# Performance work log

Hardware: AMD Instinct MI355X
Metric: run time of the kernel (lower is better)

The kernel has to match this reference:

```python
import jax, jax.numpy as jnp
import numpy as np

B, N, C = 4, 2048, 1152
H = 16
DH = C // H  # 72
EPS = 1e-6
THETA = 10000.0


def _rms_norm(x, w):
    # per-head RMSNorm in fp32, matching LlamaRMSNorm
    xf = x.astype(jnp.float32)
    var = jnp.mean(xf * xf, axis=-1, keepdims=True)
    return (w * (xf * jax.lax.rsqrt(var + EPS)).astype(x.dtype))


def _rope_cos_sin(n, dh, dtype):
    half = dh // 2
    inv_freq = 1.0 / (THETA ** (jnp.arange(0, half, dtype=jnp.float32) / half))
    ang = jnp.arange(n, dtype=jnp.float32)[:, None] * inv_freq[None, :]  # [N, half]
    return jnp.cos(ang).astype(dtype), jnp.sin(ang).astype(dtype)


def _apply_rope(x, cos, sin):
    # x: [B,H,N,DH]; rotate-half style
    half = x.shape[-1] // 2
    x1, x2 = x[..., :half], x[..., half:]
    return jnp.concatenate([x1 * cos - x2 * sin, x2 * cos + x1 * sin], axis=-1)


def setup_inputs() -> dict:
    key = jax.random.key(0)
    ks = jax.random.split(key, 3)
    x = jax.random.normal(ks[0], (B, N, C), dtype=jnp.float32)
    w_qkv = jax.random.normal(ks[1], (3 * C, C), dtype=jnp.float32) * (C ** -0.5)
    w_proj = jax.random.normal(ks[2], (C, C), dtype=jnp.float32) * (C ** -0.5)
    b_proj = jnp.zeros((C,), dtype=jnp.float32)
    q_norm_w = jnp.ones((DH,), dtype=jnp.float32)
    k_norm_w = jnp.ones((DH,), dtype=jnp.float32)
    return {"x": x, "w_qkv": w_qkv, "w_proj": w_proj, "b_proj": b_proj,
            "q_norm_w": q_norm_w, "k_norm_w": k_norm_w}


def reference(x, w_qkv, w_proj, b_proj, q_norm_w, k_norm_w):
    b, n, c = x.shape
    # QKV projection (no bias)
    qkv = jnp.einsum('bnc,dc->bnd', x, w_qkv)  # [B,N,3C]
    qkv = qkv.reshape(b, n, 3, H, DH).transpose(2, 0, 3, 1, 4)  # [3,B,H,N,DH]
    q, k, v = qkv[0], qkv[1], qkv[2]
    # RoPE on q, k
    cos, sin = _rope_cos_sin(n, DH, x.dtype)  # [N, DH/2]
    q = _apply_rope(q, cos, sin)
    k = _apply_rope(k, cos, sin)
    # per-head QK RMSNorm
    q = _rms_norm(q, q_norm_w)
    k = _rms_norm(k, k_norm_w)
    # scaled dot-product attention
    scale = DH ** -0.5
    attn = jax.nn.softmax(jnp.einsum('bhqd,bhkd->bhqk', q, k) * scale, axis=-1)
    out = jnp.einsum('bhqk,bhkd->bhqd', attn, v)  # [B,H,N,DH]
    out = out.transpose(0, 2, 1, 3).reshape(b, n, c)
    return jnp.einsum('bnc,dc->bnd', out, w_proj) + b_proj
```

## Files before the change

kernel.cpp:

```cpp
#include <hip/hip_runtime.h>
#include <stdint.h>

#define BATCH 4
#define NSEQ  2048
#define CDIM  1152
#define HB    16
#define DHD   72
#define D3    3456
#define NT    8192

typedef __attribute__((ext_vector_type(8))) short short8;
typedef __attribute__((ext_vector_type(8))) unsigned short u16x8;
typedef __attribute__((ext_vector_type(4))) unsigned short u16x4;
typedef __attribute__((ext_vector_type(4))) float f32x4;

__device__ __forceinline__ float bf2f(unsigned short u) {
  return __uint_as_float(((unsigned)u) << 16);
}
__device__ __forceinline__ unsigned short f2bf(float f) {
  unsigned u = __float_as_uint(f);
  u += 0x7FFF + ((u >> 16) & 1);
  return (unsigned short)(u >> 16);
}
__device__ __forceinline__ unsigned short f2bf_ru(float f) {
  return (unsigned short)((__float_as_uint(f) + 0x8000u) >> 16);
}

__device__ __forceinline__ void gload_lds16(const unsigned short* g, unsigned short* l) {
  __builtin_amdgcn_global_load_lds(
      (const __attribute__((address_space(1))) void*)g,
      (__attribute__((address_space(3))) void*)l, 16, 0, 0);
}

#define XN    ((size_t)NT * CDIM)
#define WQN   ((size_t)D3 * CDIM)
#define WPN   ((size_t)CDIM * CDIM)
#define CVT_CHUNKS ((XN + WQN + WPN) / 4)

__global__ __launch_bounds__(256) void cvt_bf16(
    const float* __restrict__ x, const float* __restrict__ wq,
    const float* __restrict__ wp, unsigned short* __restrict__ xb,
    unsigned short* __restrict__ wqb, unsigned short* __restrict__ wpb) {
  size_t c = (size_t)blockIdx.x * 256 + threadIdx.x;
  if (c >= CVT_CHUNKS) return;
  const float* src;
  unsigned short* dst;
  size_t e = c * 4;
  if (e < XN) { src = x + e; dst = xb + e; }
  else if (e < XN + WQN) { src = wq + (e - XN); dst = wqb + (e - XN); }
  else { src = wp + (e - XN - WQN); dst = wpb + (e - XN - WQN); }
  f32x4 v = *(const f32x4*)src;
  u16x4 r;
#pragma unroll
  for (int i = 0; i < 4; i++) r[i] = f2bf(v[i]);
  *(u16x4*)dst = r;
}

template <int SCATTER>
__global__ __launch_bounds__(256) void gemm_bt(
    const unsigned short* __restrict__ A, const unsigned short* __restrict__ Bt,
    const float* __restrict__ bias, void* __restrict__ Cout,
    unsigned short* __restrict__ Vt, int M, int Dn, int K) {
  __shared__ __attribute__((aligned(16))) unsigned short sA[128 * 32];
  __shared__ __attribute__((aligned(16))) unsigned short sB[128 * 32];

  const int tid  = threadIdx.x;
  const int lane = tid & 63;
  const int w    = tid >> 6;
  const int wm   = w >> 1, wn = w & 1;
  const int quad = lane >> 4, l16 = lane & 15;

  const int gx  = gridDim.x;
  const int nwg = gx * gridDim.y;
  const int lb  = blockIdx.y * gx + blockIdx.x;
  const int swz = (lb & 7) * (nwg >> 3) + (lb >> 3);
  const int m0 = (swz / gx) * 128, n0 = (swz % gx) * 128;

  const int srow = (lane >> 2);
  const int scol = (lane & 3) << 3;

  const f32x4 zero = {0.f, 0.f, 0.f, 0.f};
  f32x4 acc[4][4];
#pragma unroll
  for (int i = 0; i < 4; i++)
#pragma unroll
    for (int j = 0; j < 4; j++) acc[i][j] = zero;

  for (int kt = 0; kt < K; kt += 32) {
#pragma unroll
    for (int i = 0; i < 2; i++) {
      int ck = w * 2 + i;
      gload_lds16(A + (size_t)(m0 + ck * 16 + srow) * K + kt + scol, sA + ck * 512);
      gload_lds16(Bt + (size_t)(n0 + ck * 16 + srow) * K + kt + scol, sB + ck * 512);
    }
    __syncthreads();

    short8 a[4], b[4];
#pragma unroll
    for (int i = 0; i < 4; i++)
      a[i] = *(const short8*)(sA + (wm * 64 + i * 16 + l16) * 32 + quad * 8);
#pragma unroll
    for (int j = 0; j < 4; j++)
      b[j] = *(const short8*)(sB + (wn * 64 + j * 16 + l16) * 32 + quad * 8);

#pragma unroll
    for (int i = 0; i < 4; i++)
#pragma unroll
      for (int j = 0; j < 4; j++)
        acc[i][j] = __builtin_amdgcn_mfma_f32_16x16x32_bf16(a[i], b[j], acc[i][j], 0, 0, 0);
    __syncthreads();
  }

#pragma unroll
  for (int i = 0; i < 4; i++) {
    int row = m0 + wm * 64 + i * 16 + quad * 4;
#pragma unroll
    for (int j = 0; j < 4; j++) {
      int col = n0 + wn * 64 + j * 16 + l16;
      if (SCATTER) {
        int s  = col / CDIM;
        int rm = col - s * CDIM;
        int h  = rm / DHD;
        int dh = rm - h * DHD;
        int b_ = row >> 11;
        int n  = row & 2047;
        if (s == 2) {
#pragma unroll
          for (int r = 0; r < 4; r++)
            Vt[((size_t)(b_ * HB + h) * DHD + dh) * NSEQ + n + r] = f2bf(acc[i][j][r]);
        } else {
          unsigned short* Cb = (unsigned short*)Cout;
#pragma unroll
          for (int r = 0; r < 4; r++)
            Cb[(((size_t)(s * BATCH + b_) * HB + h) * NSEQ + (n + r)) * DHD + dh] =
                f2bf(acc[i][j][r]);
        }
      } else {
        float bb = bias ? bias[col] : 0.f;
        float* Cf = (float*)Cout;
#pragma unroll
        for (int r = 0; r < 4; r++)
          Cf[(size_t)(row + r) * Dn + col] = acc[i][j][r] + bb;
      }
    }
  }
}

__global__ __launch_bounds__(256) void rope_rms(
    unsigned short* __restrict__ qkvb,
    const float* __restrict__ qw, const float* __restrict__ kw) {
  const int blk = blockIdx.x;
  const int b = blk >> 11;
  const int n = blk & 2047;
  const int tid = threadIdx.x;

  __shared__ float sv[2][CDIM];
  __shared__ float srsq[2][HB];

  const float nf = (float)n;
  const float l2t_over_half = 13.287712379549449f / 36.0f;
  const float scale2 = 0.17002329230297715f;

  for (int e = tid; e < CDIM; e += 256) {
    int h  = e / DHD;
    int dh = e - h * DHD;
    int i  = (dh < 36) ? dh : dh - 36;
    float inv_freq = exp2f(-l2t_over_half * (float)i);
    float ang = nf * inv_freq;
    float sn, cs;
    __sincosf(ang, &sn, &cs);
#pragma unroll
    for (int sel = 0; sel < 2; sel++) {
      size_t ah = (((size_t)(sel * BATCH + b) * HB + h) * NSEQ + n) * DHD;
      float x1 = bf2f(qkvb[ah + i]);
      float x2 = bf2f(qkvb[ah + i + 36]);
      sv[sel][e] = (dh < 36) ? (x1 * cs - x2 * sn) : (x2 * cs + x1 * sn);
    }
  }
  __syncthreads();
  if (tid < 128) {
    int sel = tid >> 6;
    int h = (tid & 63) >> 2, p = tid & 3;
    float s = 0.f;
#pragma unroll
    for (int d = 0; d < 18; d++) {
      float v = sv[sel][h * DHD + p * 18 + d];
      s += v * v;
    }
    s += __shfl_xor(s, 1);
    s += __shfl_xor(s, 2);
    if (p == 0)
      srsq[sel][h] = rsqrtf(s * (1.0f / 72.0f) + 1e-6f) * (sel ? 1.0f : scale2);
  }
  __syncthreads();
  for (int e = tid; e < CDIM; e += 256) {
    int h  = e / DHD;
    int dh = e - h * DHD;
#pragma unroll
    for (int sel = 0; sel < 2; sel++) {
      const float* wnorm = sel ? kw : qw;
      size_t ah = (((size_t)(sel * BATCH + b) * HB + h) * NSEQ + n) * DHD;
      qkvb[ah + dh] = f2bf(sv[sel][e] * srsq[sel][h] * wnorm[dh]);
    }
  }
}

#define SPW 68
__global__ __launch_bounds__(256, 3) void flash_attn(
    const unsigned short* __restrict__ qkvb, const unsigned short* __restrict__ Vt,
    unsigned short* __restrict__ AO) {
  __shared__ __attribute__((aligned(16))) unsigned short sK[2 * 64 * 72];
  __shared__ __attribute__((aligned(16))) unsigned short sVt[80 * 64];
  __shared__ __attribute__((aligned(16))) unsigned short sP[128 * SPW];

  const int tid  = threadIdx.x;
  const int w    = tid >> 6;
  const int lane = tid & 63;
  const int quad = lane >> 4, l16 = lane & 15;
  const int q0 = blockIdx.x * 128;
  const int h = blockIdx.y, b = blockIdx.z;

  const unsigned short* Qb = qkvb + ((size_t)(0 * BATCH + b) * HB + h) * NSEQ * DHD;
  const unsigned short* Kb = qkvb + ((size_t)(1 * BATCH + b) * HB + h) * NSEQ * DHD;
  const unsigned short* Vb = Vt + (size_t)(b * HB + h) * DHD * NSEQ;

  const short8 zs = {0, 0, 0, 0, 0, 0, 0, 0};
  const f32x4 zero = {0.f, 0.f, 0.f, 0.f};

  const int vswz = ((lane & 7) ^ (lane >> 3)) * 8;
  const int iw = w;
  const unsigned short* pKn[3];
  const unsigned short* pVn[3];
#pragma unroll
  for (int j = 0; j < 3; j++) {
    int i = iw + 4 * j;
    int ii = (i < 9) ? i : 0;
    pKn[j] = Kb + ii * 512 + lane * 8;
    pVn[j] = Vb + (size_t)(ii * 8 + (lane >> 3)) * NSEQ + vswz;
  }

#pragma unroll
  for (int j = 0; j < 3; j++) {
    int i = iw + 4 * j;
    if (i < 9) {
      gload_lds16(pKn[j], sK + i * 512);
      gload_lds16(pVn[j], sVt + i * 512);
    }
  }

  for (int e = tid; e < 512; e += 256)
    sVt[72 * 64 + e] = (e < 64) ? (unsigned short)0x3F80 : (unsigned short)0;

  short8 aq[2][3];
#pragma unroll
  for (int qt = 0; qt < 2; qt++) {
    const unsigned short* qrow = Qb + (size_t)(q0 + w * 32 + qt * 16 + l16) * DHD;
    aq[qt][0] = *(const short8*)(qrow + quad * 8);
    aq[qt][1] = *(const short8*)(qrow + 32 + quad * 8);
    aq[qt][2] = (quad == 0) ? *(const short8*)(qrow + 64) : zs;
  }

  f32x4 o[2][5];
#pragma unroll
  for (int qt = 0; qt < 2; qt++)
#pragma unroll
    for (int nb = 0; nb < 5; nb++) o[qt][nb] = zero;

  auto sphase_pack = [&](const unsigned short* sKb) {
    f32x4 st[2][4];
    __builtin_amdgcn_s_setprio(1);
#pragma unroll
    for (int nk = 0; nk < 4; nk++) {
      const unsigned short* kr = sKb + (nk * 16 + l16) * 72;
      short8 kf0 = *(const short8*)(kr + quad * 8);
      short8 kf1 = *(const short8*)(kr + 32 + quad * 8);
      short8 kf2 = *(const short8*)(kr + 64);
      f32x4 s0 = zero, s1 = zero;
      s0 = __builtin_amdgcn_mfma_f32_16x16x32_bf16(kf0, aq[0][0], s0, 0, 0, 0);
      s1 = __builtin_amdgcn_mfma_f32_16x16x32_bf16(kf0, aq[1][0], s1, 0, 0, 0);
      s0 = __builtin_amdgcn_mfma_f32_16x16x32_bf16(kf1, aq[0][1], s0, 0, 0, 0);
      s1 = __builtin_amdgcn_mfma_f32_16x16x32_bf16(kf1, aq[1][1], s1, 0, 0, 0);
      s0 = __builtin_amdgcn_mfma_f32_16x16x32_bf16(kf2, aq[0][2], s0, 0, 0, 0);
      s1 = __builtin_amdgcn_mfma_f32_16x16x32_bf16(kf2, aq[1][2], s1, 0, 0, 0);
      st[0][nk] = s0;
      st[1][nk] = s1;
    }
    __builtin_amdgcn_s_setprio(0);
#pragma unroll
    for (int qt = 0; qt < 2; qt++) {
      unsigned short* prow = sP + (qt * 64 + w * 16 + l16) * SPW + quad * 4;
#pragma unroll
      for (int nk = 0; nk < 4; nk++) {
        u16x4 pr;
#pragma unroll
        for (int r = 0; r < 4; r++) pr[r] = f2bf_ru(exp2f(st[qt][nk][r]));
        *(u16x4*)(prow + nk * 16) = pr;
      }
    }
  };

  auto pv_phase = [&]() {
    __builtin_amdgcn_s_setprio(1);
#pragma unroll
    for (int kb = 0; kb < 2; kb++) {
      short8 pf0 = *(const short8*)(sP + (w * 16 + l16) * SPW + kb * 32 + quad * 8);
      short8 pf1 = *(const short8*)(sP + (64 + w * 16 + l16) * SPW + kb * 32 + quad * 8);
#pragma unroll
      for (int nb = 0; nb < 5; nb++) {
        short8 vf = *(const short8*)(sVt + (nb * 16 + l16) * 64 +
                                     ((kb * 32 + quad * 8) ^ ((l16 & 7) * 8)));
        o[0][nb] = __builtin_amdgcn_mfma_f32_16x16x32_bf16(pf0, vf, o[0][nb], 0, 0, 0);
        o[1][nb] = __builtin_amdgcn_mfma_f32_16x16x32_bf16(pf1, vf, o[1][nb], 0, 0, 0);
      }
    }
    __builtin_amdgcn_s_setprio(0);
  };

  __syncthreads();

#pragma unroll
  for (int j = 0; j < 3; j++) {
    int i = iw + 4 * j;
    if (i < 9) gload_lds16(pKn[j] + 64 * 72, sK + 4608 + i * 512);
    pKn[j] += 2 * 64 * 72;
  }

  sphase_pack(sK);
  __syncthreads();

  for (int t = 0; t < 32; t++) {
    pv_phase();

    if (t < 31) {
      __syncthreads();

#pragma unroll
      for (int j = 0; j < 3; j++) {
        int i = iw + 4 * j;
        if (i < 9) gload_lds16(pVn[j] + 64, sVt + i * 512);
        pVn[j] += 64;
      }
      if (t < 30) {
#pragma unroll
        for (int j = 0; j < 3; j++) {
          int i = iw + 4 * j;
          if (i < 9) gload_lds16(pKn[j], sK + (t & 1) * 4608 + i * 512);
          pKn[j] += 64 * 72;
        }
      }

      sphase_pack(sK + ((t + 1) & 1) * 4608);
      __syncthreads();
    }
  }

#pragma unroll
  for (int qt = 0; qt < 2; qt++) {
    float inv[4];
#pragma unroll
    for (int r = 0; r < 4; r++)
      inv[r] = 1.0f / __shfl(o[qt][4][r], (quad << 4) + 8, 64);
    const int qrow = q0 + w * 32 + qt * 16 + quad * 4;
#pragma unroll
    for (int nb = 0; nb < 5; nb++) {
      int dh = nb * 16 + l16;
      if (dh < DHD) {
#pragma unroll
        for (int r = 0; r < 4; r++)
          AO[((size_t)b * NSEQ + qrow + r) * CDIM + h * DHD + dh] =
              f2bf(o[qt][nb][r] * inv[r]);
      }
    }
  }
}

extern "C" void kernel_launch(void* const* d_in, const int* in_sizes, int n_in,
                              void* d_out, int out_size, void* d_ws, size_t ws_size,
                              hipStream_t stream) {
  const float* x      = (const float*)d_in[0];
  const float* w_qkv  = (const float*)d_in[1];
  const float* w_proj = (const float*)d_in[2];
  const float* b_proj = (const float*)d_in[3];
  const float* qnw    = (const float*)d_in[4];
  const float* knw    = (const float*)d_in[5];
  float* out = (float*)d_out;

  char* ws = (char*)d_ws;
  unsigned short* xb    = (unsigned short*)(ws);
  unsigned short* wqkvb = (unsigned short*)(ws + 18874368);
  unsigned short* wprojb= (unsigned short*)(ws + 26836992);
  unsigned short* qkvb  = (unsigned short*)(ws + 29491200);
  unsigned short* Vt    = (unsigned short*)(ws + 67239936);
  unsigned short* AO    = xb;

  cvt_bf16<<<dim3((CVT_CHUNKS + 255) / 256), 256, 0, stream>>>(
      x, w_qkv, w_proj, xb, wqkvb, wprojb);
  gemm_bt<1><<<dim3(D3 / 128, NT / 128), 256, 0, stream>>>(
      xb, wqkvb, nullptr, qkvb, Vt, NT, D3, CDIM);
  rope_rms<<<dim3(NT), 256, 0, stream>>>(qkvb, qnw, knw);
  flash_attn<<<dim3(NSEQ / 128, HB, BATCH), 256, 0, stream>>>(qkvb, Vt, AO);
  gemm_bt<0><<<dim3(CDIM / 128, NT / 128), 256, 0, stream>>>(
      AO, wprojb, b_proj, out, nullptr, NT, CDIM, CDIM);
}
```

Measured before the change: 395.8 us.

## Single-buffer K in flash attention, swizzle P tile, raise occupancy to 4 blocks

Drops K double-buffering and the padded P stride, which shrinks LDS use so launch bounds can ask for 4 blocks per CU instead of 3. The P tile now uses an XOR swizzle instead of padding to avoid bank conflicts. Packing to bf16 now uses the v_cvt_pk_bf16_f32 instruction instead of manual round-up. The loop is reordered so the S-phase, the K load and the PV-phase are separated by two barriers per iteration. This gives up the overlap of the next K load with the current compute and adds more barrier stalls, in exchange for more resident waves.

```diff
diff --git a/kernel.cpp b/kernel.cpp
--- a/kernel.cpp
+++ b/kernel.cpp
@@ -12,6 +12,7 @@
 typedef __attribute__((ext_vector_type(8))) short short8;
 typedef __attribute__((ext_vector_type(8))) unsigned short u16x8;
 typedef __attribute__((ext_vector_type(4))) unsigned short u16x4;
+typedef __attribute__((ext_vector_type(2))) unsigned int u32x2;
 typedef __attribute__((ext_vector_type(4))) float f32x4;
 
 __device__ __forceinline__ float bf2f(unsigned short u) {
@@ -22,8 +23,10 @@
   u += 0x7FFF + ((u >> 16) & 1);
   return (unsigned short)(u >> 16);
 }
-__device__ __forceinline__ unsigned short f2bf_ru(float f) {
-  return (unsigned short)((__float_as_uint(f) + 0x8000u) >> 16);
+__device__ __forceinline__ unsigned pkbf(float lo, float hi) {
+  unsigned r;
+  asm("v_cvt_pk_bf16_f32 %0, %1, %2" : "=v"(r) : "v"(lo), "v"(hi));
+  return r;
 }
 
 __device__ __forceinline__ void gload_lds16(const unsigned short* g, unsigned short* l) {
@@ -205,18 +208,18 @@
   }
 }
 
-#define SPW 68
-__global__ __launch_bounds__(256, 3) void flash_attn(
+__global__ __launch_bounds__(256, 4) void flash_attn(
     const unsigned short* __restrict__ qkvb, const unsigned short* __restrict__ Vt,
     unsigned short* __restrict__ AO) {
-  __shared__ __attribute__((aligned(16))) unsigned short sK[2 * 64 * 72];
+  __shared__ __attribute__((aligned(16))) unsigned short sK[64 * 72];
   __shared__ __attribute__((aligned(16))) unsigned short sVt[80 * 64];
-  __shared__ __attribute__((aligned(16))) unsigned short sP[128 * SPW];
+  __shared__ __attribute__((aligned(16))) unsigned short sP[128 * 64];
 
   const int tid  = threadIdx.x;
   const int w    = tid >> 6;
   const int lane = tid & 63;
   const int quad = lane >> 4, l16 = lane & 15;
+  const int s7   = l16 & 7;
   const int q0 = blockIdx.x * 128;
   const int h = blockIdx.y, b = blockIdx.z;
 
@@ -228,12 +231,11 @@
   const f32x4 zero = {0.f, 0.f, 0.f, 0.f};
 
   const int vswz = ((lane & 7) ^ (lane >> 3)) * 8;
-  const int iw = w;
   const unsigned short* pKn[3];
   const unsigned short* pVn[3];
 #pragma unroll
   for (int j = 0; j < 3; j++) {
-    int i = iw + 4 * j;
+    int i = w + 4 * j;
     int ii = (i < 9) ? i : 0;
     pKn[j] = Kb + ii * 512 + lane * 8;
     pVn[j] = Vb + (size_t)(ii * 8 + (lane >> 3)) * NSEQ + vswz;
@@ -241,10 +243,12 @@
 
 #pragma unroll
   for (int j = 0; j < 3; j++) {
-    int i = iw + 4 * j;
+    int i = w + 4 * j;
     if (i < 9) {
       gload_lds16(pKn[j], sK + i * 512);
       gload_lds16(pVn[j], sVt + i * 512);
+      pKn[j] += 64 * 72;
+      pVn[j] += 64;
     }
   }
 
@@ -266,12 +270,12 @@
 #pragma unroll
     for (int nb = 0; nb < 5; nb++) o[qt][nb] = zero;
 
-  auto sphase_pack = [&](const unsigned short* sKb) {
+  auto sphase_pack = [&]() {
     f32x4 st[2][4];
     __builtin_amdgcn_s_setprio(1);
 #pragma unroll
     for (int nk = 0; nk < 4; nk++) {
-      const unsigned short* kr = sKb + (nk * 16 + l16) * 72;
+      const unsigned short* kr = sK + (nk * 16 + l16) * 72;
       short8 kf0 = *(const short8*)(kr + quad * 8);
       short8 kf1 = *(const short8*)(kr + 32 + quad * 8);
       short8 kf2 = *(const short8*)(kr + 64);
@@ -288,13 +292,14 @@
     __builtin_amdgcn_s_setprio(0);
 #pragma unroll
     for (int qt = 0; qt < 2; qt++) {
-      unsigned short* prow = sP + (qt * 64 + w * 16 + l16) * SPW + quad * 4;
+      unsigned short* prow = sP + (qt * 64 + w * 16 + l16) * 64 + (quad & 1) * 4;
 #pragma unroll
       for (int nk = 0; nk < 4; nk++) {
-        u16x4 pr;
-#pragma unroll
-        for (int r = 0; r < 4; r++) pr[r] = f2bf_ru(exp2f(st[qt][nk][r]));
-        *(u16x4*)(prow + nk * 16) = pr;
+        int uoff = ((nk * 2 + (quad >> 1)) ^ s7) << 3;
+        u32x2 pr;
+        pr[0] = pkbf(exp2f(st[qt][nk][0]), exp2f(st[qt][nk][1]));
+        pr[1] = pkbf(exp2f(st[qt][nk][2]), exp2f(st[qt][nk][3]));
+        *(u32x2*)(prow + uoff) = pr;
       }
     }
   };
@@ -303,12 +308,14 @@
     __builtin_amdgcn_s_setprio(1);
 #pragma unroll
     for (int kb = 0; kb < 2; kb++) {
-      short8 pf0 = *(const short8*)(sP + (w * 16 + l16) * SPW + kb * 32 + quad * 8);
-      short8 pf1 = *(const short8*)(sP + (64 + w * 16 + l16) * SPW + kb * 32 + quad * 8);
+      const unsigned short* pp =
+          sP + (w * 16 + l16) * 64 + (((kb * 4 + quad) ^ s7) << 3);
+      short8 pf0 = *(const short8*)pp;
+      short8 pf1 = *(const short8*)(pp + 64 * 64);
 #pragma unroll
       for (int nb = 0; nb < 5; nb++) {
         short8 vf = *(const short8*)(sVt + (nb * 16 + l16) * 64 +
-                                     ((kb * 32 + quad * 8) ^ ((l16 & 7) * 8)));
+                                     (((kb * 4 + quad) ^ s7) << 3));
         o[0][nb] = __builtin_amdgcn_mfma_f32_16x16x32_bf16(pf0, vf, o[0][nb], 0, 0, 0);
         o[1][nb] = __builtin_amdgcn_mfma_f32_16x16x32_bf16(pf1, vf, o[1][nb], 0, 0, 0);
       }
@@ -318,39 +325,29 @@
 
   __syncthreads();
 
-#pragma unroll
-  for (int j = 0; j < 3; j++) {
-    int i = iw + 4 * j;
-    if (i < 9) gload_lds16(pKn[j] + 64 * 72, sK + 4608 + i * 512);
-    pKn[j] += 2 * 64 * 72;
-  }
-
-  sphase_pack(sK);
-  __syncthreads();
-
   for (int t = 0; t < 32; t++) {
+    sphase_pack();
+
+    __syncthreads();
+
+    if (t < 31) {
+#pragma unroll
+      for (int j = 0; j < 3; j++) {
+        int i = w + 4 * j;
+        if (i < 9) { gload_lds16(pKn[j], sK + i * 512); pKn[j] += 64 * 72; }
+      }
+    }
+
     pv_phase();
 
+    __syncthreads();
+
     if (t < 31) {
-      __syncthreads();
-
 #pragma unroll
       for (int j = 0; j < 3; j++) {
-        int i = iw + 4 * j;
-        if (i < 9) gload_lds16(pVn[j] + 64, sVt + i * 512);
-        pVn[j] += 64;
-      }
-      if (t < 30) {
-#pragma unroll
-        for (int j = 0; j < 3; j++) {
-          int i = iw + 4 * j;
-          if (i < 9) gload_lds16(pKn[j], sK + (t & 1) * 4608 + i * 512);
-          pKn[j] += 64 * 72;
-        }
-      }
-
-      sphase_pack(sK + ((t + 1) & 1) * 4608);
-      __syncthreads();
+        int i = w + 4 * j;
+        if (i < 9) { gload_lds16(pVn[j], sVt + i * 512); pVn[j] += 64; }
+      }
     }
   }
 
```

Result: no change. 393.8 us (-0.5%).
